# Kernel optimization log

Measured on AMD Instinct MI355X. Metric: run time of the kernel, lower is better.

Reference implementation:

```python
import jax, jax.numpy as jnp
import numpy as np

DIM = 1024
NUM_HEADS = 16
HEAD_DIM = DIM // NUM_HEADS  # 64
GRID = 32                    # ft_seq_len = pt_seq_len = 32 -> seq_len = 1024
ROPE_DIM = HEAD_DIM // 2     # 32; repeat_interleave(2)+concat -> 64 = head_dim
EPS = 1e-6


def _rope_tables():
    theta = 10000.0
    freqs = 1.0 / theta ** (np.arange(0, ROPE_DIM, 2, dtype=np.float32) / ROPE_DIM)  # [16]
    positions = np.arange(GRID, dtype=np.float32) / GRID * GRID                      # [32]
    f = np.einsum('n,d->nd', positions, freqs)                                       # [32,16]
    f = np.repeat(f, 2, axis=-1)                                                     # [32,32]
    f2 = np.concatenate([np.broadcast_to(f[:, None, :], (GRID, GRID, ROPE_DIM)),
                         np.broadcast_to(f[None, :, :], (GRID, GRID, ROPE_DIM))],
                        axis=-1).reshape(GRID * GRID, 2 * ROPE_DIM)                  # [1024,64]
    return np.cos(f2).astype(np.float32), np.sin(f2).astype(np.float32)


def setup_inputs() -> dict:
    key = jax.random.key(0)
    ks = jax.random.split(key, 8)
    B, S = 8, GRID * GRID
    cos_np, sin_np = _rope_tables()
    s = 0.02
    return {
        'hidden_states': jax.random.normal(ks[0], (B, S, DIM), jnp.float32),
        'W_qkv': jax.random.normal(ks[1], (DIM, 3 * DIM), jnp.float32) * s,
        'b_qkv': jnp.zeros((3 * DIM,), jnp.float32),
        'qn_w': jnp.ones((HEAD_DIM,), jnp.float32),
        'qn_b': jnp.zeros((HEAD_DIM,), jnp.float32),
        'kn_w': jnp.ones((HEAD_DIM,), jnp.float32),
        'kn_b': jnp.zeros((HEAD_DIM,), jnp.float32),
        'W_proj': jax.random.normal(ks[2], (DIM, DIM), jnp.float32) * s,
        'b_proj': jnp.zeros((DIM,), jnp.float32),
        'freqs_cos': jnp.asarray(cos_np),
        'freqs_sin': jnp.asarray(sin_np),
    }


def _rotate_half(x):
    x2 = x.reshape(*x.shape[:-1], -1, 2)
    a, b = x2[..., 0], x2[..., 1]
    return jnp.stack((-b, a), axis=-1).reshape(x.shape)


def _layernorm(x, w, b):
    mu = jnp.mean(x, axis=-1, keepdims=True)
    var = jnp.mean(jnp.square(x - mu), axis=-1, keepdims=True)
    return (x - mu) * jax.lax.rsqrt(var + EPS) * w + b


def reference(hidden_states, W_qkv, b_qkv, qn_w, qn_b, kn_w, kn_b, W_proj, b_proj, freqs_cos, freqs_sin):
    B, S, C = hidden_states.shape
    qkv = hidden_states @ W_qkv + b_qkv                               # [B,S,3C]
    qkv = qkv.reshape(B, S, 3, NUM_HEADS, HEAD_DIM).transpose(2, 0, 3, 1, 4)
    q, k, v = qkv[0], qkv[1], qkv[2]                                  # [B,H,S,D]
    q = _layernorm(q, qn_w, qn_b)
    k = _layernorm(k, kn_w, kn_b)
    # RoPE: cos/sin broadcast over batch and heads; tables are [S, D]
    q = q * freqs_cos + _rotate_half(q) * freqs_sin
    k = k * freqs_cos + _rotate_half(k) * freqs_sin
    scale = 1.0 / jnp.sqrt(jnp.asarray(HEAD_DIM, q.dtype))
    scores = jnp.einsum('bhqd,bhkd->bhqk', q, k) * scale
    attn = jax.nn.softmax(scores, axis=-1)
    out = jnp.einsum('bhqk,bhkd->bhqd', attn, v)                      # [B,H,S,D]
    out = out.transpose(0, 2, 1, 3).reshape(B, S, C)
    return out @ W_proj + b_proj
```

## Files before the change

kernel.cpp:

```cpp
#include <hip/hip_runtime.h>
#include <hip/hip_bf16.h>

#define DEV __device__ __forceinline__

typedef __attribute__((ext_vector_type(8))) short bf16x8;
typedef __attribute__((ext_vector_type(4))) short short4v;
typedef __attribute__((ext_vector_type(4))) float f32x4;
typedef __attribute__((ext_vector_type(4))) int int4v;

static constexpr int BATCH = 8;
static constexpr int SEQ   = 1024;
static constexpr int CDIM  = 1024;
static constexpr int NH    = 16;
static constexpr int HD    = 64;
static constexpr int N3    = 3072;

DEV short f2bf(float x) {
    __hip_bfloat16 h = __float2bfloat16(x);
    return __builtin_bit_cast(short, h);
}
DEV float bf2f(short x) {
    unsigned u = ((unsigned)(unsigned short)x) << 16;
    return __builtin_bit_cast(float, u);
}
DEV float exp2_hw(float x) {
    float r;
    asm("v_exp_f32 %0, %1" : "=v"(r) : "v"(x));
    return r;
}

typedef __attribute__((address_space(1))) const unsigned gas_u32;
typedef __attribute__((address_space(3))) unsigned las_u32;
DEV void gll16(const void* g, void* l) {
    __builtin_amdgcn_global_load_lds((gas_u32*)g, (las_u32*)l, 16, 0, 0);
}

__global__ __launch_bounds__(256) void k_prep(
    const float* __restrict__ hidden, short* __restrict__ hbf,
    const float* __restrict__ Wq, short* __restrict__ WqT,
    const float* __restrict__ Wp, short* __restrict__ WpT) {
    __shared__ float tile[32][33];
    int bid = blockIdx.x, tid = threadIdx.x;
    if (bid < 4096) {
        int i = (bid * 256 + tid) * 8;
        float4 a = *(const float4*)(hidden + i);
        float4 b = *(const float4*)(hidden + i + 4);
        bf16x8 o;
        o[0] = f2bf(a.x); o[1] = f2bf(a.y); o[2] = f2bf(a.z); o[3] = f2bf(a.w);
        o[4] = f2bf(b.x); o[5] = f2bf(b.y); o[6] = f2bf(b.z); o[7] = f2bf(b.w);
        *(bf16x8*)(hbf + i) = o;
        return;
    }
    const float* src; short* dst; int K, N, bx, by;
    if (bid < 4096 + 3072) {
        int bt = bid - 4096; src = Wq; dst = WqT; K = CDIM; N = N3;
        bx = bt % (N3 / 32); by = bt / (N3 / 32);
    } else {
        int bt = bid - 7168; src = Wp; dst = WpT; K = CDIM; N = CDIM;
        bx = bt % (CDIM / 32); by = bt / (CDIM / 32);
    }
    int tx = tid & 31, ty = tid >> 5;
    int n0 = bx * 32, k0 = by * 32;
    for (int i = 0; i < 32; i += 8)
        tile[ty + i][tx] = src[(size_t)(k0 + ty + i) * N + n0 + tx];
    __syncthreads();
    for (int i = 0; i < 32; i += 8)
        dst[(size_t)(n0 + ty + i) * K + k0 + tx] = f2bf(tile[tx][ty + i]);
}

template <bool OUT_BF16>
__global__ __launch_bounds__(512, 2) void k_gemmA(
    const short* __restrict__ A, const short* __restrict__ Bt,
    const float* __restrict__ bias, void* __restrict__ Cout,
    int M, int N, int K) {
    __shared__ char lds[2][3][16384];
    const int tid = threadIdx.x;
    const int wid = tid >> 6, l = tid & 63;
    const int lr = l & 15, lk = l >> 4;
    const int wm = wid >> 2, wn = wid & 3;
    const int nbn = N >> 7;
    const int nwg = gridDim.x;
    const int q8 = nwg >> 3;
    const int wg = (blockIdx.x & 7) * q8 + (blockIdx.x >> 3);
    const int m0 = (wg / nbn) << 8, n0 = (wg % nbn) << 7;
    const int NT = K >> 6;

    auto stA = [&](int buf, int h, int kt) {
#pragma unroll
        for (int j = 0; j < 2; ++j) {
            int L = (wid * 64 + l + j * 512) * 16;
            int b = L ^ (((L >> 7) & 7) << 4);
            int hr = b >> 7, ke = (b & 127) >> 1;
            int grow = m0 + (hr & 63) + h * 64 + ((hr >> 6) << 7);
            gll16(A + (size_t)grow * K + kt * 64 + ke,
                  &lds[buf][h][wid * 1024 + j * 8192]);
        }
    };
    auto stB = [&](int buf, int kt) {
#pragma unroll
        for (int j = 0; j < 2; ++j) {
            int L = (wid * 64 + l + j * 512) * 16;
            int b = L ^ (((L >> 7) & 7) << 4);
            int hr = b >> 7, ke = (b & 127) >> 1;
            int grow = n0 + hr;
            gll16(Bt + (size_t)grow * K + kt * 64 + ke,
                  &lds[buf][2][wid * 1024 + j * 8192]);
        }
    };
    auto rdA = [&](int buf, int h, int mi, int ks) -> bf16x8 {
        int b = (wm * 64 + mi * 16 + lr) * 128 + ks * 64 + lk * 16;
        return *(const bf16x8*)&lds[buf][h][b ^ (((b >> 7) & 7) << 4)];
    };
    auto rdB = [&](int buf, int ni, int ks) -> bf16x8 {
        int b = (wn * 32 + ni * 16 + lr) * 128 + ks * 64 + lk * 16;
        return *(const bf16x8*)&lds[buf][2][b ^ (((b >> 7) & 7) << 4)];
    };

    f32x4 acc[8][2] = {};
    stA(0, 0, 0); stB(0, 0); stA(0, 1, 0);
    stA(1, 0, 1); stB(1, 1);
    asm volatile("s_waitcnt vmcnt(4)" ::: "memory");
    __builtin_amdgcn_s_barrier();

    bf16x8 aF[4][2], bB[2][2];
    for (int T = 0; T < NT; ++T) {
        const int p = T & 1;
#pragma unroll
        for (int ni = 0; ni < 2; ++ni) { bB[ni][0] = rdB(p, ni, 0); bB[ni][1] = rdB(p, ni, 1); }
#pragma unroll
        for (int mi = 0; mi < 4; ++mi) { aF[mi][0] = rdA(p, 0, mi, 0); aF[mi][1] = rdA(p, 0, mi, 1); }
        if (T + 1 < NT) stA(p ^ 1, 1, T + 1);
        __builtin_amdgcn_s_barrier();
        asm volatile("s_waitcnt lgkmcnt(0)" ::: "memory");
        __builtin_amdgcn_s_setprio(1);
#pragma unroll
        for (int mi = 0; mi < 4; ++mi)
#pragma unroll
            for (int ni = 0; ni < 2; ++ni)
#pragma unroll
                for (int ks = 0; ks < 2; ++ks)
                    acc[mi][ni] = __builtin_amdgcn_mfma_f32_16x16x32_bf16(aF[mi][ks], bB[ni][ks], acc[mi][ni], 0, 0, 0);
        __builtin_amdgcn_s_setprio(0);
        __builtin_amdgcn_s_barrier();
#pragma unroll
        for (int mi = 0; mi < 4; ++mi) { aF[mi][0] = rdA(p, 1, mi, 0); aF[mi][1] = rdA(p, 1, mi, 1); }
        if (T + 2 < NT) {
            stA(p, 0, T + 2); stB(p, T + 2);
            asm volatile("s_waitcnt vmcnt(4)" ::: "memory");
        } else {
            asm volatile("s_waitcnt vmcnt(0)" ::: "memory");
        }
        __builtin_amdgcn_s_barrier();
        asm volatile("s_waitcnt lgkmcnt(0)" ::: "memory");
        __builtin_amdgcn_s_setprio(1);
#pragma unroll
        for (int mi = 0; mi < 4; ++mi)
#pragma unroll
            for (int ni = 0; ni < 2; ++ni)
#pragma unroll
                for (int ks = 0; ks < 2; ++ks)
                    acc[4 + mi][ni] = __builtin_amdgcn_mfma_f32_16x16x32_bf16(aF[mi][ks], bB[ni][ks], acc[4 + mi][ni], 0, 0, 0);
        __builtin_amdgcn_s_setprio(0);
        __builtin_amdgcn_s_barrier();
    }
#pragma unroll
    for (int ami = 0; ami < 8; ++ami) {
        int grow = m0 + wm * 128 + (ami >> 2) * 64 + (ami & 3) * 16 + lk * 4;
#pragma unroll
        for (int ani = 0; ani < 2; ++ani) {
            int gcol = n0 + wn * 32 + ani * 16 + lr;
            float bv = bias[gcol];
#pragma unroll
            for (int r = 0; r < 4; ++r) {
                float v = acc[ami][ani][r] + bv;
                if (OUT_BF16) ((short*)Cout)[(size_t)(grow + r) * N + gcol] = f2bf(v);
                else          ((float*)Cout)[(size_t)(grow + r) * N + gcol] = v;
            }
        }
    }
}

__global__ __launch_bounds__(256) void k_lnrope_vt(
    const short* __restrict__ qkv,
    const float* __restrict__ qn_w, const float* __restrict__ qn_b,
    const float* __restrict__ kn_w, const float* __restrict__ kn_b,
    const float* __restrict__ fcos, const float* __restrict__ fsin,
    short* __restrict__ q, short* __restrict__ k, short* __restrict__ vt) {
    __shared__ short tile[64][72];
    int bid = blockIdx.x, tid = threadIdx.x;
    if (bid < 8192) {
        int l = tid & 63;
        int gw = bid * 4 + (tid >> 6);
        int job = gw * 8 + (l >> 3);
        int sub = l & 7;
        int h = job & 15;
        int t = job >> 4;
        int which = t & 1;
        int bs = t >> 1;
        int s = bs & 1023, b = bs >> 10;
        bf16x8 xv = *(const bf16x8*)(qkv + (size_t)bs * N3 + which * CDIM + h * HD + sub * 8);
        float x[8];
#pragma unroll
        for (int j = 0; j < 8; ++j) x[j] = bf2f(xv[j]);
        float sum = 0.f;
#pragma unroll
        for (int j = 0; j < 8; ++j) sum += x[j];
        sum += __shfl_xor(sum, 1); sum += __shfl_xor(sum, 2); sum += __shfl_xor(sum, 4);
        float mu = sum * (1.f / 64.f);
        float var = 0.f;
#pragma unroll
        for (int j = 0; j < 8; ++j) { x[j] -= mu; var += x[j] * x[j]; }
        var += __shfl_xor(var, 1); var += __shfl_xor(var, 2); var += __shfl_xor(var, 4);
        float rs = rsqrtf(var * (1.f / 64.f) + 1e-6f);
        const float* wv = which ? kn_w : qn_w;
        const float* bb = which ? kn_b : qn_b;
        float wl[8], bl[8], cl[8], sl[8];
        *(float4*)&wl[0] = *(const float4*)(wv + sub * 8);
        *(float4*)&wl[4] = *(const float4*)(wv + sub * 8 + 4);
        *(float4*)&bl[0] = *(const float4*)(bb + sub * 8);
        *(float4*)&bl[4] = *(const float4*)(bb + sub * 8 + 4);
        *(float4*)&cl[0] = *(const float4*)(fcos + s * HD + sub * 8);
        *(float4*)&cl[4] = *(const float4*)(fcos + s * HD + sub * 8 + 4);
        *(float4*)&sl[0] = *(const float4*)(fsin + s * HD + sub * 8);
        *(float4*)&sl[4] = *(const float4*)(fsin + s * HD + sub * 8 + 4);
        float y[8];
#pragma unroll
        for (int j = 0; j < 8; ++j) y[j] = x[j] * rs * wl[j] + bl[j];
        bf16x8 ov;
#pragma unroll
        for (int j = 0; j < 8; j += 2) {
            float e = y[j] * cl[j] - y[j + 1] * sl[j];
            float o = y[j + 1] * cl[j + 1] + y[j] * sl[j + 1];
            ov[j] = f2bf(e); ov[j + 1] = f2bf(o);
        }
        short* dst = which ? k : q;
        *(bf16x8*)(dst + ((size_t)(b * NH + h) * SEQ + s) * HD + sub * 8) = ov;
        return;
    }
    int vb = bid - 8192;
    int st = vb & 15, bh = vb >> 4;
    int h = bh & 15, b = bh >> 4;
    int s0 = st * 64;
    const short* src = qkv + (size_t)b * SEQ * N3 + 2 * CDIM + h * HD;
    for (int c = tid; c < 512; c += 256) {
        int sr = c >> 3, cg = c & 7;
        *(int4v*)&tile[sr][cg * 8] = *(const int4v*)&src[(size_t)(s0 + sr) * N3 + cg * 8];
    }
    __syncthreads();
    short* dst = vt + (size_t)bh * HD * SEQ + s0;
    for (int c = tid; c < 512; c += 256) {
        int d = c >> 3, sg = c & 7;
        short tmp[8];
#pragma unroll
        for (int j = 0; j < 8; ++j) tmp[j] = tile[sg * 8 + j][d];
        *(int4v*)&dst[(size_t)d * SEQ + sg * 8] = *(const int4v*)tmp;
    }
}

__global__ __launch_bounds__(512, 4) void k_attn(
    const short* __restrict__ q, const short* __restrict__ k, const short* __restrict__ vt,
    short* __restrict__ out ) {
    constexpr int KVB = 64;
    constexpr int NT = SEQ / KVB;
    __shared__ short Ks[2][KVB * 64];
    __shared__ short Vs[2][64 * KVB];
    int tid = threadIdx.x, w = tid >> 6, l = tid & 63;
    int bid = blockIdx.x;
    int swz = (bid & 7) * 64 + (bid >> 3);
    int bh = swz >> 2;
    int q0 = (swz & 3) * 256;
    const short* qb = q  + (size_t)bh * SEQ * HD;
    const short* kb = k  + (size_t)bh * SEQ * HD;
    const short* vb = vt + (size_t)bh * HD * SEQ;
    int lr = l & 15, lk = l >> 4;
    bf16x8 qB[2][2];
#pragma unroll
    for (int f = 0; f < 2; ++f) {
        int qrow = q0 + f * 128 + w * 16 + lr;
        qB[f][0] = *(const bf16x8*)&qb[(size_t)qrow * HD + lk * 8];
        qB[f][1] = *(const bf16x8*)&qb[(size_t)qrow * HD + 32 + lk * 8];
    }
    f32x4 accO[2][4] = {};
    float ls_acc[2] = {0.f, 0.f};
    int g0 = 2 * (lk & 1);
    bool hi = (lk >> 1) != 0;
    constexpr float SC2 = 0.125f * 1.44269504f;

    int srow = tid >> 3, scg = tid & 7;
    int soff = srow * 128 + ((scg * 16) ^ ((srow & 7) << 4));
    const short* kg = kb + (size_t)srow * HD + scg * 8;
    const short* vg = vb + (size_t)srow * SEQ + scg * 8;
    int4v kreg = *(const int4v*)kg;
    int4v vreg = *(const int4v*)vg;
    *(int4v*)((char*)Ks[0] + soff) = kreg;
    *(int4v*)((char*)Vs[0] + soff) = vreg;

    for (int t = 0; t < NT; ++t) {
        __syncthreads();
        int cur = t & 1;
        if (t + 1 < NT) {
            kreg = *(const int4v*)(kg + (size_t)(t + 1) * KVB * HD);
            vreg = *(const int4v*)(vg + (t + 1) * KVB);
        }
        f32x4 sc[2][4];
        __builtin_amdgcn_s_setprio(1);
#pragma unroll
        for (int nf = 0; nf < 4; ++nf) {
            int row = nf * 16 + lr;
            f32x4 a0 = {}, a1 = {};
#pragma unroll
            for (int ks = 0; ks < 2; ++ks) {
                bf16x8 kf = *(const bf16x8*)((const char*)Ks[cur] + row * 128 +
                                             ((ks * 64 + lk * 16) ^ ((row & 7) << 4)));
                a0 = __builtin_amdgcn_mfma_f32_16x16x32_bf16(kf, qB[0][ks], a0, 0, 0, 0);
                a1 = __builtin_amdgcn_mfma_f32_16x16x32_bf16(kf, qB[1][ks], a1, 0, 0, 0);
            }
            sc[0][nf] = a0; sc[1][nf] = a1;
        }
        __builtin_amdgcn_s_setprio(0);
        unsigned pwd[2][4][2];
#pragma unroll
        for (int f = 0; f < 2; ++f) {
            float lsf = ls_acc[f];
#pragma unroll
            for (int nf = 0; nf < 4; ++nf) {
                float p0 = exp2_hw(sc[f][nf][0] * SC2);
                float p1 = exp2_hw(sc[f][nf][1] * SC2);
                float p2 = exp2_hw(sc[f][nf][2] * SC2);
                float p3 = exp2_hw(sc[f][nf][3] * SC2);
                lsf += (p0 + p1) + (p2 + p3);
                pwd[f][nf][0] = (unsigned)(unsigned short)f2bf(p0) |
                                ((unsigned)(unsigned short)f2bf(p1) << 16);
                pwd[f][nf][1] = (unsigned)(unsigned short)f2bf(p2) |
                                ((unsigned)(unsigned short)f2bf(p3) << 16);
            }
            ls_acc[f] = lsf;
        }
#pragma unroll
        for (int c = 0; c < 2; ++c) {
            bf16x8 pf[2];
#pragma unroll
            for (int f = 0; f < 2; ++f) {
                unsigned wds[4];
#pragma unroll
                for (int w2 = 0; w2 < 4; ++w2) {
                    int src = lr + 16 * (g0 + (w2 >> 1));
                    unsigned a0 = (unsigned)__shfl((int)pwd[f][2 * c][w2 & 1], src);
                    unsigned a1 = (unsigned)__shfl((int)pwd[f][2 * c + 1][w2 & 1], src);
                    wds[w2] = hi ? a1 : a0;
                }
                int4v wi = { (int)wds[0], (int)wds[1], (int)wds[2], (int)wds[3] };
                pf[f] = __builtin_bit_cast(bf16x8, wi);
            }
            __builtin_amdgcn_s_setprio(1);
#pragma unroll
            for (int df = 0; df < 4; ++df) {
                int row = df * 16 + lr;
                bf16x8 vf = *(const bf16x8*)((const char*)Vs[cur] + row * 128 +
                                             ((c * 64 + lk * 16) ^ ((row & 7) << 4)));
                accO[0][df] = __builtin_amdgcn_mfma_f32_16x16x32_bf16(vf, pf[0], accO[0][df], 0, 0, 0);
                accO[1][df] = __builtin_amdgcn_mfma_f32_16x16x32_bf16(vf, pf[1], accO[1][df], 0, 0, 0);
            }
            __builtin_amdgcn_s_setprio(0);
        }
        if (t + 1 < NT) {
            *(int4v*)((char*)Ks[cur ^ 1] + soff) = kreg;
            *(int4v*)((char*)Vs[cur ^ 1] + soff) = vreg;
        }
    }
    int b = bh >> 4, h = bh & 15;
#pragma unroll
    for (int f = 0; f < 2; ++f) {
        float lsum = ls_acc[f];
        lsum += __shfl_xor(lsum, 16);
        lsum += __shfl_xor(lsum, 32);
        float inv = 1.f / lsum;
        int qg = q0 + f * 128 + w * 16 + lr;
#pragma unroll
        for (int df = 0; df < 4; ++df) {
            short4v o4;
#pragma unroll
            for (int r = 0; r < 4; ++r) o4[r] = f2bf(accO[f][df][r] * inv);
            *(short4v*)&out[((size_t)(b * SEQ + qg)) * CDIM + h * HD + df * 16 + lk * 4] = o4;
        }
    }
}

extern "C" void kernel_launch(void* const* d_in, const int* in_sizes, int n_in,
                              void* d_out, int out_size, void* d_ws, size_t ws_size,
                              hipStream_t stream) {
    const float* hidden = (const float*)d_in[0];
    const float* W_qkv  = (const float*)d_in[1];
    const float* b_qkv  = (const float*)d_in[2];
    const float* qn_w   = (const float*)d_in[3];
    const float* qn_b   = (const float*)d_in[4];
    const float* kn_w   = (const float*)d_in[5];
    const float* kn_b   = (const float*)d_in[6];
    const float* W_proj = (const float*)d_in[7];
    const float* b_proj = (const float*)d_in[8];
    const float* fcos   = (const float*)d_in[9];
    const float* fsin   = (const float*)d_in[10];
    float* out = (float*)d_out;

    const size_t SZ_HBF    = (size_t)BATCH * SEQ * CDIM * 2;
    const size_t SZ_WQKVT  = (size_t)N3 * CDIM * 2;
    const size_t SZ_WPROJT = (size_t)CDIM * CDIM * 2;
    const size_t SZ_QKV    = (size_t)BATCH * SEQ * N3 * 2;
    const size_t SZ_HEAD   = (size_t)BATCH * NH * SEQ * HD * 2;

    char* ws = (char*)d_ws;
    short* hbf    = (short*)ws; ws += SZ_HBF;
    short* wqkvT  = (short*)ws; ws += SZ_WQKVT;
    short* wprojT = (short*)ws; ws += SZ_WPROJT;
    short* qkv    = (short*)ws; ws += SZ_QKV;
    short* qh     = (short*)ws; ws += SZ_HEAD;
    short* kh     = (short*)ws; ws += SZ_HEAD;
    short* vt     = (short*)ws; ws += SZ_HEAD;
    short* attn_o = hbf;

    size_t needed = SZ_HBF + SZ_WQKVT + SZ_WPROJT + SZ_QKV + 3 * SZ_HEAD;
    if (ws_size < needed) return;

    k_prep<<<4096 + 3072 + 1024, 256, 0, stream>>>(hidden, hbf, W_qkv, wqkvT, W_proj, wprojT);

    k_gemmA<true><<<(BATCH * SEQ / 256) * (N3 / 128), 512, 0, stream>>>(
        hbf, wqkvT, b_qkv, qkv, BATCH * SEQ, N3, CDIM);

    k_lnrope_vt<<<8192 + 2048, 256, 0, stream>>>(
        qkv, qn_w, qn_b, kn_w, kn_b, fcos, fsin, qh, kh, vt);

    k_attn<<<BATCH * NH * (SEQ / 256), 512, 0, stream>>>(qh, kh, vt, attn_o);

    k_gemmA<false><<<(BATCH * SEQ / 256) * (CDIM / 128), 512, 0, stream>>>(
        attn_o, wprojT, b_proj, out, BATCH * SEQ, CDIM, CDIM);
}
```

Before: 182.5 us.

## Retile GEMM warps to 4x2 layout with 64x64 per-wave tiles

New measurement: 185.5 us. About the same (+1.6%).

```diff
diff --git a/kernel.cpp b/kernel.cpp
--- a/kernel.cpp
+++ b/kernel.cpp
@@ -77,7 +77,7 @@
     const int tid = threadIdx.x;
     const int wid = tid >> 6, l = tid & 63;
     const int lr = l & 15, lk = l >> 4;
-    const int wm = wid >> 2, wn = wid & 3;
+    const int wm = wid >> 1, wn = wid & 1;
     const int nbn = N >> 7;
     const int nwg = gridDim.x;
     const int q8 = nwg >> 3;
@@ -107,72 +107,72 @@
                   &lds[buf][2][wid * 1024 + j * 8192]);
         }
     };
-    auto rdA = [&](int buf, int h, int mi, int ks) -> bf16x8 {
-        int b = (wm * 64 + mi * 16 + lr) * 128 + ks * 64 + lk * 16;
-        return *(const bf16x8*)&lds[buf][h][b ^ (((b >> 7) & 7) << 4)];
+    auto rdA = [&](int buf, int mi, int ks) -> bf16x8 {
+        int b = ((wm >> 1) * 64 + mi * 16 + lr) * 128 + ks * 64 + lk * 16;
+        return *(const bf16x8*)&lds[buf][wm & 1][b ^ (((b >> 7) & 7) << 4)];
     };
     auto rdB = [&](int buf, int ni, int ks) -> bf16x8 {
-        int b = (wn * 32 + ni * 16 + lr) * 128 + ks * 64 + lk * 16;
+        int b = (wn * 64 + ni * 16 + lr) * 128 + ks * 64 + lk * 16;
         return *(const bf16x8*)&lds[buf][2][b ^ (((b >> 7) & 7) << 4)];
     };
 
-    f32x4 acc[8][2] = {};
+    f32x4 acc[4][4] = {};
     stA(0, 0, 0); stB(0, 0); stA(0, 1, 0);
     stA(1, 0, 1); stB(1, 1);
     asm volatile("s_waitcnt vmcnt(4)" ::: "memory");
     __builtin_amdgcn_s_barrier();
 
-    bf16x8 aF[4][2], bB[2][2];
+    bf16x8 aF[4], bF[4];
     for (int T = 0; T < NT; ++T) {
         const int p = T & 1;
 #pragma unroll
-        for (int ni = 0; ni < 2; ++ni) { bB[ni][0] = rdB(p, ni, 0); bB[ni][1] = rdB(p, ni, 1); }
-#pragma unroll
-        for (int mi = 0; mi < 4; ++mi) { aF[mi][0] = rdA(p, 0, mi, 0); aF[mi][1] = rdA(p, 0, mi, 1); }
+        for (int mi = 0; mi < 4; ++mi) aF[mi] = rdA(p, mi, 0);
+#pragma unroll
+        for (int ni = 0; ni < 4; ++ni) bF[ni] = rdB(p, ni, 0);
+        asm volatile("s_waitcnt lgkmcnt(0)" ::: "memory");
+        __builtin_amdgcn_sched_barrier(0);
+        __builtin_amdgcn_s_barrier();
         if (T + 1 < NT) stA(p ^ 1, 1, T + 1);
-        __builtin_amdgcn_s_barrier();
-        asm volatile("s_waitcnt lgkmcnt(0)" ::: "memory");
         __builtin_amdgcn_s_setprio(1);
 #pragma unroll
         for (int mi = 0; mi < 4; ++mi)
 #pragma unroll
-            for (int ni = 0; ni < 2; ++ni)
-#pragma unroll
-                for (int ks = 0; ks < 2; ++ks)
-                    acc[mi][ni] = __builtin_amdgcn_mfma_f32_16x16x32_bf16(aF[mi][ks], bB[ni][ks], acc[mi][ni], 0, 0, 0);
+            for (int ni = 0; ni < 4; ++ni)
+                acc[mi][ni] = __builtin_amdgcn_mfma_f32_16x16x32_bf16(aF[mi], bF[ni], acc[mi][ni], 0, 0, 0);
         __builtin_amdgcn_s_setprio(0);
         __builtin_amdgcn_s_barrier();
 #pragma unroll
-        for (int mi = 0; mi < 4; ++mi) { aF[mi][0] = rdA(p, 1, mi, 0); aF[mi][1] = rdA(p, 1, mi, 1); }
+        for (int mi = 0; mi < 4; ++mi) aF[mi] = rdA(p, mi, 1);
+#pragma unroll
+        for (int ni = 0; ni < 4; ++ni) bF[ni] = rdB(p, ni, 1);
+        asm volatile("s_waitcnt lgkmcnt(0)" ::: "memory");
+        __builtin_amdgcn_sched_barrier(0);
+        __builtin_amdgcn_s_barrier();
+        if (T + 2 < NT) { stA(p, 0, T + 2); stB(p, T + 2); }
+        __builtin_amdgcn_s_setprio(1);
+#pragma unroll
+        for (int mi = 0; mi < 4; ++mi)
+#pragma unroll
+            for (int ni = 0; ni < 4; ++ni)
+                acc[mi][ni] = __builtin_amdgcn_mfma_f32_16x16x32_bf16(aF[mi], bF[ni], acc[mi][ni], 0, 0, 0);
+        __builtin_amdgcn_s_setprio(0);
         if (T + 2 < NT) {
-            stA(p, 0, T + 2); stB(p, T + 2);
             asm volatile("s_waitcnt vmcnt(4)" ::: "memory");
         } else {
             asm volatile("s_waitcnt vmcnt(0)" ::: "memory");
         }
         __builtin_amdgcn_s_barrier();
-        asm volatile("s_waitcnt lgkmcnt(0)" ::: "memory");
-        __builtin_amdgcn_s_setprio(1);
-#pragma unroll
-        for (int mi = 0; mi < 4; ++mi)
-#pragma unroll
-            for (int ni = 0; ni < 2; ++ni)
-#pragma unroll
-                for (int ks = 0; ks < 2; ++ks)
-                    acc[4 + mi][ni] = __builtin_amdgcn_mfma_f32_16x16x32_bf16(aF[mi][ks], bB[ni][ks], acc[4 + mi][ni], 0, 0, 0);
-        __builtin_amdgcn_s_setprio(0);
-        __builtin_amdgcn_s_barrier();
-    }
-#pragma unroll
-    for (int ami = 0; ami < 8; ++ami) {
-        int grow = m0 + wm * 128 + (ami >> 2) * 64 + (ami & 3) * 16 + lk * 4;
-#pragma unroll
-        for (int ani = 0; ani < 2; ++ani) {
-            int gcol = n0 + wn * 32 + ani * 16 + lr;
+    }
+#pragma unroll
+    for (int mi = 0; mi < 4; ++mi) {
+        int grow = m0 + wm * 64 + mi * 16 + lk * 4;
+#pragma unroll
+        for (int ni = 0; ni < 4; ++ni) {
+            int gcol = n0 + wn * 64 + ni * 16 + lr;
             float bv = bias[gcol];
 #pragma unroll
             for (int r = 0; r < 4; ++r) {
-                float v = acc[ami][ani][r] + bv;
+                float v = acc[mi][ni][r] + bv;
                 if (OUT_BF16) ((short*)Cout)[(size_t)(grow + r) * N + gcol] = f2bf(v);
                 else          ((float*)Cout)[(size_t)(grow + r) * N + gcol] = v;
             }
```
